# Performance work log

Hardware: AMD Instinct MI355X
Metric: run time of the kernel (lower is better)

The kernel has to match this reference:

```python
import jax, jax.numpy as jnp
import numpy as np

EMBED_DIM = 1024
NUM_HEADS = 16
HEAD_DIM = EMBED_DIM // NUM_HEADS


def setup_inputs() -> dict:
    key = jax.random.key(0)
    ks = jax.random.split(key, 5)
    s = 0.02
    return {
        "x": jax.random.normal(ks[0], (2, 2048, EMBED_DIM), dtype=jnp.float32),
        "w_qkv": jax.random.normal(ks[1], (EMBED_DIM, 3 * EMBED_DIM), dtype=jnp.float32) * s,
        "b_qkv": jnp.zeros((3 * EMBED_DIM,), dtype=jnp.float32),
        "w_out": jax.random.normal(ks[2], (EMBED_DIM, EMBED_DIM), dtype=jnp.float32) * s,
        "b_out": jnp.zeros((EMBED_DIM,), dtype=jnp.float32),
    }


def reference(x, w_qkv, b_qkv, w_out, b_out):
    B, T, C = x.shape
    qkv = x @ w_qkv + b_qkv                       # [B,T,3C]
    q, k, v = jnp.split(qkv, 3, axis=-1)
    # [B,T,C] -> [B,H,T,Dh]
    def heads(t):
        return t.reshape(B, T, NUM_HEADS, HEAD_DIM).transpose(0, 2, 1, 3)
    q, k, v = heads(q), heads(k), heads(v)
    scale = 1.0 / np.sqrt(HEAD_DIM).astype(np.float32)
    scores = jnp.einsum("bhqd,bhkd->bhqk", q, k) * scale  # [B,H,T,T]
    causal = jnp.tril(jnp.ones((T, T), dtype=bool))
    scores = jnp.where(causal[None, None], scores, -jnp.inf)
    attn = jax.nn.softmax(scores, axis=-1)
    out = jnp.einsum("bhqk,bhkd->bhqd", attn, v)  # [B,H,T,Dh]
    out = out.transpose(0, 2, 1, 3).reshape(B, T, C)
    return out @ w_out + b_out
```

## Files before the change

### kernel.cpp

```cpp
#include <hip/hip_runtime.h>

typedef unsigned short u16;
typedef unsigned int u32;
typedef __attribute__((ext_vector_type(2))) unsigned int u32x2;
typedef __attribute__((ext_vector_type(8))) short bf16x8;
typedef __attribute__((ext_vector_type(4))) float f32x4;
typedef __attribute__((ext_vector_type(16))) float f32x16;

#define TOK   4096
#define EMB   1024
#define NQKV  3072
#define TSEQ  2048
#define NH    16

__device__ __forceinline__ u16 f2b(float f) {
  union { float f; unsigned u; } v; v.f = f;
  unsigned r = v.u + 0x7FFFu + ((v.u >> 16) & 1u);
  return (u16)(r >> 16);
}

__device__ __forceinline__ u16 f2b_hu(float f) {
  return (u16)((__float_as_uint(f) + 0x8000u) >> 16);
}

__device__ __forceinline__ u32 pack_rn(float a, float b) {
  u32 ua = __float_as_uint(a) + 0x8000u;
  u32 ub = __float_as_uint(b) + 0x8000u;
  return __builtin_amdgcn_perm(ub, ua, 0x07060302u);
}

__device__ __forceinline__ f32x16 zero16() {
  f32x16 z;
#pragma unroll
  for (int i = 0; i < 16; i++) z[i] = 0.f;
  return z;
}

__device__ __forceinline__ void gload16(const void* g, void* l) {
  __builtin_amdgcn_global_load_lds((const __attribute__((address_space(1))) void*)g,
                                   (__attribute__((address_space(3))) void*)l, 16, 0, 0);
}


__global__ __launch_bounds__(256) void prep_kernel(const float* __restrict__ x,
                                                   u16* __restrict__ x_bf,
                                                   const float* __restrict__ w_qkv,
                                                   u16* __restrict__ wqkvT,
                                                   const float* __restrict__ w_out,
                                                   u16* __restrict__ woutT) {
  __shared__ u16 sm[64][65];
  int bid = blockIdx.x, tid = threadIdx.x;
  if (bid < 4096) {
    int i = bid * 256 + tid;
    float4 v = ((const float4*)x)[i];
    union { u16 us[4]; uint2 u2; } o;
    o.us[0] = f2b(v.x); o.us[1] = f2b(v.y); o.us[2] = f2b(v.z); o.us[3] = f2b(v.w);
    ((uint2*)x_bf)[i] = o.u2;
    return;
  }
  const float* src; u16* dst; int R, C, bx, by;
  if (bid < 4096 + 768) {
    int t = bid - 4096; bx = t % 48; by = t / 48;
    src = w_qkv; dst = wqkvT; R = EMB; C = NQKV;
  } else {
    int t = bid - 4096 - 768; bx = t & 15; by = t >> 4;
    src = w_out; dst = woutT; R = EMB; C = EMB;
  }
  int c0 = bx * 64, r0 = by * 64;
#pragma unroll
  for (int i = 0; i < 16; i++) {
    int idx = tid + i * 256;
    int r = idx >> 6, c = idx & 63;
    sm[r][c] = f2b(src[(size_t)(r0 + r) * C + c0 + c]);
  }
  __syncthreads();
  int cc2 = tid >> 2, rr0 = (tid & 3) * 16;
  union { u16 us[16]; uint4 v4[2]; } o;
#pragma unroll
  for (int j = 0; j < 16; j++) o.us[j] = sm[rr0 + j][cc2];
  *(uint4*)&dst[(size_t)(c0 + cc2) * R + r0 + rr0]     = o.v4[0];
  *(uint4*)&dst[(size_t)(c0 + cc2) * R + r0 + rr0 + 8] = o.v4[1];
}


template <int MODE, int TN, int CW, int CH>
__global__ __launch_bounds__(256) void gemm_bt(const u16* __restrict__ A,
                                               const u16* __restrict__ Bt,
                                               const float* __restrict__ bias,
                                               u16* __restrict__ qb, u16* __restrict__ kb,
                                               u16* __restrict__ vb, float* __restrict__ outp,
                                               int K, int N) {
  constexpr int CT = TN / 32;
  constexpr int RB = TN / 32;
  __shared__ u16 As[2][128][64];
  __shared__ u16 Bs[2][TN][64];
  int tid = threadIdx.x;
  int bx, by;
  if constexpr (CW > 0) {
    int bid = blockIdx.x;
    int xcd = bid & 7, idx = bid >> 3;
    bx = (xcd & 1) * CW + idx % CW;
    by = (xcd >> 1) * CH + idx / CW;
  } else {
    bx = blockIdx.x; by = blockIdx.y;
  }
  int m0 = by * 128, n0 = bx * TN;
  int lane = tid & 63, wid = tid >> 6;
  int wm = (wid >> 1) * 64;
  int wn = (wid & 1) * (TN / 2);
  int l15 = lane & 15, quad = lane >> 4;
  int srow = lane >> 3;
  int scol = (((lane & 7) ^ srow) * 8);

  f32x4 acc[4][CT];
#pragma unroll
  for (int i = 0; i < 4; i++)
#pragma unroll
    for (int j = 0; j < CT; j++) acc[i][j] = (f32x4){0.f, 0.f, 0.f, 0.f};

  const u16* Ag = A + (size_t)(m0 + wid * 32 + srow) * K + scol;
  const u16* Bg = Bt + (size_t)(n0 + wid * (TN / 4) + srow) * K + scol;

#pragma unroll
  for (int i = 0; i < 4; i++)
    gload16(Ag + (size_t)(i * 8) * K, &As[0][wid * 32 + i * 8][0]);
#pragma unroll
  for (int i = 0; i < RB; i++)
    gload16(Bg + (size_t)(i * 8) * K, &Bs[0][wid * (TN / 4) + i * 8][0]);
  __syncthreads();

  int cur = 0;
  for (int k0 = 0; k0 < K; k0 += 64) {
    if (k0 + 64 < K) {
      int kn = k0 + 64;
#pragma unroll
      for (int i = 0; i < 4; i++)
        gload16(Ag + (size_t)(i * 8) * K + kn, &As[cur ^ 1][wid * 32 + i * 8][0]);
#pragma unroll
      for (int i = 0; i < RB; i++)
        gload16(Bg + (size_t)(i * 8) * K + kn, &Bs[cur ^ 1][wid * (TN / 4) + i * 8][0]);
    }

#pragma unroll
    for (int ks = 0; ks < 2; ks++) {
      bf16x8 af[4], bfr[CT];
#pragma unroll
      for (int rt = 0; rt < 4; rt++)
        af[rt] = *(const bf16x8*)&As[cur][wm + rt * 16 + l15][((ks * 4 + quad) ^ (l15 & 7)) * 8];
#pragma unroll
      for (int ct = 0; ct < CT; ct++)
        bfr[ct] = *(const bf16x8*)&Bs[cur][wn + ct * 16 + l15][((ks * 4 + quad) ^ (l15 & 7)) * 8];
#pragma unroll
      for (int rt = 0; rt < 4; rt++)
#pragma unroll
        for (int ct = 0; ct < CT; ct++)
          acc[rt][ct] = __builtin_amdgcn_mfma_f32_16x16x32_bf16(bfr[ct], af[rt], acc[rt][ct], 0, 0, 0);
    }
    __syncthreads();
    cur ^= 1;
  }

#pragma unroll
  for (int rt = 0; rt < 4; rt++) {
#pragma unroll
    for (int ct = 0; ct < CT; ct++) {
      int m = m0 + wm + rt * 16 + l15;
      int nb = n0 + wn + ct * 16 + quad * 4;
      float4 b4 = *(const float4*)&bias[nb];
      float v0 = acc[rt][ct][0] + b4.x, v1 = acc[rt][ct][1] + b4.y;
      float v2 = acc[rt][ct][2] + b4.z, v3 = acc[rt][ct][3] + b4.w;
      if (MODE == 0) {
        int sel = nb >> 10;
        int c = nb & 1023;
        int h = c >> 6, d0 = c & 63;
        int b = m >> 11, t = m & 2047;
        if (sel == 2) {
          size_t vbase = ((((size_t)b * NH + h) * 64 + d0) * TSEQ) + t;
          vb[vbase]            = f2b_hu(v0);
          vb[vbase + TSEQ]     = f2b_hu(v1);
          vb[vbase + 2 * TSEQ] = f2b_hu(v2);
          vb[vbase + 3 * TSEQ] = f2b_hu(v3);
        } else {
          u16* dst = sel ? kb : qb;
          union { u32 u[2]; uint2 u2; } o;
          o.u[0] = pack_rn(v0, v1);
          o.u[1] = pack_rn(v2, v3);
          *(uint2*)&dst[((((size_t)b * NH + h) * TSEQ + t) << 6) + d0] = o.u2;
        }
      } else {
        float4 o = {v0, v1, v2, v3};
        *(float4*)&outp[(size_t)m * N + nb] = o;
      }
    }
  }
}


__global__ __launch_bounds__(256, 4) void attn_kernel(const u16* __restrict__ Qb,
                                                      const u16* __restrict__ Kb,
                                                      const u16* __restrict__ Vtb,
                                                      u16* __restrict__ O) {
  __shared__ u16 Ks[64][68];
  __shared__ u16 Vt[64][68];
  __shared__ float Cmb[2][16][64][2];
  __shared__ float Lmb[2][32];

  const float SCL = 0.18033688f;
  const float MOFF = 16.0f;

  int phys = blockIdx.x;
  int xcd = phys & 7;
  int cuL = (phys >> 3) & 31;
  int slot = phys >> 8;
  int bh = xcd * 4 + slot;
  int qt = (slot & 1) ? (31 - cuL) : cuL;

  int tid = threadIdx.x, lane = tid & 63, w = tid >> 6;
  int sub = w & 1, par = w >> 1;
  int l31 = lane & 31, h = lane >> 5;
  const size_t hoff = (size_t)bh * TSEQ * 64;

  int qw = qt * 64 + sub * 32;
  int qg = qw + l31;

  bf16x8 qf[4];
  {
    const u16* qp = Qb + hoff + (size_t)qg * 64 + h * 8;
#pragma unroll
    for (int s = 0; s < 4; s++) qf[s] = *(const bf16x8*)(qp + s * 16);
  }

  f32x16 acc[2];
  acc[0] = zero16(); acc[1] = zero16();
  float l_i = 0.f;

  int r = tid >> 2, cb = (tid & 3) * 16;
  bf16x8 kr0, kr1, vr0, vr1;
  {
    const u16* kg = Kb + hoff + (size_t)r * 64 + cb;
    const u16* vg = Vtb + hoff + (size_t)r * TSEQ + cb;
    kr0 = *(const bf16x8*)kg;       kr1 = *(const bf16x8*)(kg + 8);
    vr0 = *(const bf16x8*)vg;       vr1 = *(const bf16x8*)(vg + 8);
  }

  for (int kt = 0; kt <= qt; kt++) {
    __syncthreads();
    *(bf16x8*)&Ks[r][cb]     = kr0;
    *(bf16x8*)&Ks[r][cb + 8] = kr1;
    *(bf16x8*)&Vt[r][cb]     = vr0;
    *(bf16x8*)&Vt[r][cb + 8] = vr1;
    __syncthreads();
    if (kt < qt) {
      const u16* kg = Kb + hoff + (size_t)((kt + 1) * 64 + r) * 64 + cb;
      const u16* vg = Vtb + hoff + (size_t)r * TSEQ + (kt + 1) * 64 + cb;
      kr0 = *(const bf16x8*)kg;     kr1 = *(const bf16x8*)(kg + 8);
      vr0 = *(const bf16x8*)vg;     vr1 = *(const bf16x8*)(vg + 8);
    }

    int kbt = kt * 64 + par * 32;
    if (kbt <= qw + 31) {
      f32x16 sacc = zero16();
      __builtin_amdgcn_s_setprio(1);
#pragma unroll
      for (int s = 0; s < 4; s++) {
        bf16x8 kf = *(const bf16x8*)&Ks[par * 32 + l31][s * 16 + h * 8];
        sacc = __builtin_amdgcn_mfma_f32_32x32x16_bf16(kf, qf[s], sacc, 0, 0, 0);
      }
      __builtin_amdgcn_s_setprio(0);

      if (kbt + 31 > qw) {
#pragma unroll
        for (int rr = 0; rr < 16; rr++) {
          int key = kbt + (rr & 3) + 8 * (rr >> 2) + 4 * h;
          if (key > qg) sacc[rr] = -1e30f;
        }
      }

#pragma unroll
      for (int rr = 0; rr < 16; rr++) {
        float p = exp2f(__builtin_fmaf(sacc[rr], SCL, -MOFF));
        sacc[rr] = p;
        l_i += p;
      }

#pragma unroll
      for (int s2 = 0; s2 < 2; s2++) {
        u32 u0, u1, u2, u3;
        asm("v_cvt_pk_bf16_f32 %0, %1, %2" : "=v"(u0) : "v"(sacc[8 * s2 + 0]), "v"(sacc[8 * s2 + 1]));
        asm("v_cvt_pk_bf16_f32 %0, %1, %2" : "=v"(u1) : "v"(sacc[8 * s2 + 2]), "v"(sacc[8 * s2 + 3]));
        asm("v_cvt_pk_bf16_f32 %0, %1, %2" : "=v"(u2) : "v"(sacc[8 * s2 + 4]), "v"(sacc[8 * s2 + 5]));
        asm("v_cvt_pk_bf16_f32 %0, %1, %2" : "=v"(u3) : "v"(sacc[8 * s2 + 6]), "v"(sacc[8 * s2 + 7]));
        u32x2 r02 = __builtin_amdgcn_permlane32_swap(u0, u2, false, false);
        u32x2 r13 = __builtin_amdgcn_permlane32_swap(u1, u3, false, false);
        union { u32 d[4]; bf16x8 v; } pf;
        pf.d[0] = r02[0];
        pf.d[1] = r13[0];
        pf.d[2] = r02[1];
        pf.d[3] = r13[1];
        __builtin_amdgcn_s_setprio(1);
#pragma unroll
        for (int dt = 0; dt < 2; dt++) {
          bf16x8 vf = *(const bf16x8*)&Vt[dt * 32 + l31][par * 32 + s2 * 16 + h * 8];
          acc[dt] = __builtin_amdgcn_mfma_f32_32x32x16_bf16(vf, pf.v, acc[dt], 0, 0, 0);
        }
        __builtin_amdgcn_s_setprio(0);
      }
    }
  }

  l_i += __shfl_xor(l_i, 32);

  __syncthreads();
  if (par == 1) {
#pragma unroll
    for (int dt = 0; dt < 2; dt++)
#pragma unroll
      for (int pr = 0; pr < 8; pr++) {
        Cmb[sub][dt * 8 + pr][lane][0] = acc[dt][2 * pr];
        Cmb[sub][dt * 8 + pr][lane][1] = acc[dt][2 * pr + 1];
      }
    if (h == 0) Lmb[sub][l31] = l_i;
  }
  __syncthreads();
  if (par == 0) {
#pragma unroll
    for (int dt = 0; dt < 2; dt++)
#pragma unroll
      for (int pr = 0; pr < 8; pr++) {
        acc[dt][2 * pr]     += Cmb[sub][dt * 8 + pr][lane][0];
        acc[dt][2 * pr + 1] += Cmb[sub][dt * 8 + pr][lane][1];
      }
    float lt = l_i + Lmb[sub][l31];
    float inv = 1.0f / lt;

    int b = bh >> 4, head = bh & 15;
    size_t rowbase = ((size_t)b * TSEQ + qg) * 1024 + head * 64;
#pragma unroll
    for (int dt = 0; dt < 2; dt++)
#pragma unroll
      for (int G = 0; G < 4; G++) {
        union { u32 u[2]; uint2 u2; } o;
        o.u[0] = pack_rn(acc[dt][4 * G + 0] * inv, acc[dt][4 * G + 1] * inv);
        o.u[1] = pack_rn(acc[dt][4 * G + 2] * inv, acc[dt][4 * G + 3] * inv);
        *(uint2*)&O[rowbase + dt * 32 + G * 8 + 4 * h] = o.u2;
      }
  }
}


extern "C" void kernel_launch(void* const* d_in, const int* in_sizes, int n_in,
                              void* d_out, int out_size, void* d_ws, size_t ws_size,
                              hipStream_t stream) {
  (void)in_sizes; (void)n_in; (void)out_size; (void)ws_size;
  const float* x     = (const float*)d_in[0];
  const float* w_qkv = (const float*)d_in[1];
  const float* b_qkv = (const float*)d_in[2];
  const float* w_out = (const float*)d_in[3];
  const float* b_out = (const float*)d_in[4];
  float* out = (float*)d_out;

  char* p = (char*)d_ws;
  u16* x_bf  = (u16*)p; p += (size_t)TOK * EMB * 2;
  u16* wqkvT = (u16*)p; p += (size_t)NQKV * EMB * 2;
  u16* woutT = (u16*)p; p += (size_t)EMB * EMB * 2;
  u16* Qb    = (u16*)p; p += (size_t)32 * TSEQ * 64 * 2;
  u16* Kb    = (u16*)p; p += (size_t)32 * TSEQ * 64 * 2;
  u16* Vtb   = (u16*)p; p += (size_t)32 * TSEQ * 64 * 2;
  u16* attn_o = (u16*)p;

  prep_kernel<<<dim3(4096 + 768 + 256), 256, 0, stream>>>(x, x_bf, w_qkv, wqkvT, w_out, woutT);
  gemm_bt<0, 128, 12, 8><<<dim3(768), 256, 0, stream>>>(x_bf, wqkvT, b_qkv,
                                                        Qb, Kb, Vtb, nullptr, EMB, NQKV);
  attn_kernel<<<dim3(1024), 256, 0, stream>>>(Qb, Kb, Vtb, attn_o);
  gemm_bt<1, 64, 0, 0><<<dim3(EMB / 64, TOK / 128), 256, 0, stream>>>(attn_o, woutT, b_out,
                                                                      nullptr, nullptr, nullptr, out, EMB, EMB);
}
```

Baseline: 182.7 us.

## Double-buffer K/V tiles in LDS to drop one barrier per iteration

The attention kernel moves from a single LDS buffer for the K and V tiles to two buffers, unioned with the final combine scratch. Each iteration writes the next tile into the spare buffer and issues global loads two tiles ahead, so only one __syncthreads is needed per step. The row-sum accumulation is also split into four partial accumulators to shorten the dependent add chain. LDS use per block roughly doubles for the K/V part, which could limit occupancy under the 4-blocks-per-CU launch bound, and it keeps more registers live.

```diff
diff --git a/kernel.cpp b/kernel.cpp
--- a/kernel.cpp
+++ b/kernel.cpp
@@ -200,10 +200,10 @@
                                                       const u16* __restrict__ Kb,
                                                       const u16* __restrict__ Vtb,
                                                       u16* __restrict__ O) {
-  __shared__ u16 Ks[64][68];
-  __shared__ u16 Vt[64][68];
-  __shared__ float Cmb[2][16][64][2];
-  __shared__ float Lmb[2][32];
+  __shared__ union __align__(16) SM {
+    struct { u16 Ks[2][64][68]; u16 Vt[2][64][68]; } kv;
+    struct { float Cmb[2][16][64][2]; float Lmb[2][32]; } cb;
+  } sm;
 
   const float SCL = 0.18033688f;
   const float MOFF = 16.0f;
@@ -232,27 +232,40 @@
 
   f32x16 acc[2];
   acc[0] = zero16(); acc[1] = zero16();
-  float l_i = 0.f;
+  float lp0 = 0.f, lp1 = 0.f, lp2 = 0.f, lp3 = 0.f;
 
   int r = tid >> 2, cb = (tid & 3) * 16;
   bf16x8 kr0, kr1, vr0, vr1;
+
   {
     const u16* kg = Kb + hoff + (size_t)r * 64 + cb;
     const u16* vg = Vtb + hoff + (size_t)r * TSEQ + cb;
     kr0 = *(const bf16x8*)kg;       kr1 = *(const bf16x8*)(kg + 8);
     vr0 = *(const bf16x8*)vg;       vr1 = *(const bf16x8*)(vg + 8);
+    *(bf16x8*)&sm.kv.Ks[0][r][cb]     = kr0;
+    *(bf16x8*)&sm.kv.Ks[0][r][cb + 8] = kr1;
+    *(bf16x8*)&sm.kv.Vt[0][r][cb]     = vr0;
+    *(bf16x8*)&sm.kv.Vt[0][r][cb + 8] = vr1;
+    if (qt >= 1) {
+      const u16* kg1 = Kb + hoff + (size_t)(64 + r) * 64 + cb;
+      const u16* vg1 = Vtb + hoff + (size_t)r * TSEQ + 64 + cb;
+      kr0 = *(const bf16x8*)kg1;    kr1 = *(const bf16x8*)(kg1 + 8);
+      vr0 = *(const bf16x8*)vg1;    vr1 = *(const bf16x8*)(vg1 + 8);
+    }
   }
 
   for (int kt = 0; kt <= qt; kt++) {
     __syncthreads();
-    *(bf16x8*)&Ks[r][cb]     = kr0;
-    *(bf16x8*)&Ks[r][cb + 8] = kr1;
-    *(bf16x8*)&Vt[r][cb]     = vr0;
-    *(bf16x8*)&Vt[r][cb + 8] = vr1;
-    __syncthreads();
-    if (kt < qt) {
-      const u16* kg = Kb + hoff + (size_t)((kt + 1) * 64 + r) * 64 + cb;
-      const u16* vg = Vtb + hoff + (size_t)r * TSEQ + (kt + 1) * 64 + cb;
+    int cur = kt & 1;
+    if (kt + 1 <= qt) {
+      *(bf16x8*)&sm.kv.Ks[cur ^ 1][r][cb]     = kr0;
+      *(bf16x8*)&sm.kv.Ks[cur ^ 1][r][cb + 8] = kr1;
+      *(bf16x8*)&sm.kv.Vt[cur ^ 1][r][cb]     = vr0;
+      *(bf16x8*)&sm.kv.Vt[cur ^ 1][r][cb + 8] = vr1;
+    }
+    if (kt + 2 <= qt) {
+      const u16* kg = Kb + hoff + (size_t)((kt + 2) * 64 + r) * 64 + cb;
+      const u16* vg = Vtb + hoff + (size_t)r * TSEQ + (kt + 2) * 64 + cb;
       kr0 = *(const bf16x8*)kg;     kr1 = *(const bf16x8*)(kg + 8);
       vr0 = *(const bf16x8*)vg;     vr1 = *(const bf16x8*)(vg + 8);
     }
@@ -263,7 +276,7 @@
       __builtin_amdgcn_s_setprio(1);
 #pragma unroll
       for (int s = 0; s < 4; s++) {
-        bf16x8 kf = *(const bf16x8*)&Ks[par * 32 + l31][s * 16 + h * 8];
+        bf16x8 kf = *(const bf16x8*)&sm.kv.Ks[cur][par * 32 + l31][s * 16 + h * 8];
         sacc = __builtin_amdgcn_mfma_f32_32x32x16_bf16(kf, qf[s], sacc, 0, 0, 0);
       }
       __builtin_amdgcn_s_setprio(0);
@@ -280,7 +293,10 @@
       for (int rr = 0; rr < 16; rr++) {
         float p = exp2f(__builtin_fmaf(sacc[rr], SCL, -MOFF));
         sacc[rr] = p;
-        l_i += p;
+        if ((rr & 3) == 0)      lp0 += p;
+        else if ((rr & 3) == 1) lp1 += p;
+        else if ((rr & 3) == 2) lp2 += p;
+        else                    lp3 += p;
       }
 
 #pragma unroll
@@ -300,7 +316,7 @@
         __builtin_amdgcn_s_setprio(1);
 #pragma unroll
         for (int dt = 0; dt < 2; dt++) {
-          bf16x8 vf = *(const bf16x8*)&Vt[dt * 32 + l31][par * 32 + s2 * 16 + h * 8];
+          bf16x8 vf = *(const bf16x8*)&sm.kv.Vt[cur][dt * 32 + l31][par * 32 + s2 * 16 + h * 8];
           acc[dt] = __builtin_amdgcn_mfma_f32_32x32x16_bf16(vf, pf.v, acc[dt], 0, 0, 0);
         }
         __builtin_amdgcn_s_setprio(0);
@@ -308,6 +324,7 @@
     }
   }
 
+  float l_i = (lp0 + lp1) + (lp2 + lp3);
   l_i += __shfl_xor(l_i, 32);
 
   __syncthreads();
@@ -316,10 +333,10 @@
     for (int dt = 0; dt < 2; dt++)
 #pragma unroll
       for (int pr = 0; pr < 8; pr++) {
-        Cmb[sub][dt * 8 + pr][lane][0] = acc[dt][2 * pr];
-        Cmb[sub][dt * 8 + pr][lane][1] = acc[dt][2 * pr + 1];
-      }
-    if (h == 0) Lmb[sub][l31] = l_i;
+        sm.cb.Cmb[sub][dt * 8 + pr][lane][0] = acc[dt][2 * pr];
+        sm.cb.Cmb[sub][dt * 8 + pr][lane][1] = acc[dt][2 * pr + 1];
+      }
+    if (h == 0) sm.cb.Lmb[sub][l31] = l_i;
   }
   __syncthreads();
   if (par == 0) {
@@ -327,10 +344,10 @@
     for (int dt = 0; dt < 2; dt++)
 #pragma unroll
       for (int pr = 0; pr < 8; pr++) {
-        acc[dt][2 * pr]     += Cmb[sub][dt * 8 + pr][lane][0];
-        acc[dt][2 * pr + 1] += Cmb[sub][dt * 8 + pr][lane][1];
-      }
-    float lt = l_i + Lmb[sub][l31];
+        acc[dt][2 * pr]     += sm.cb.Cmb[sub][dt * 8 + pr][lane][0];
+        acc[dt][2 * pr + 1] += sm.cb.Cmb[sub][dt * 8 + pr][lane][1];
+      }
+    float lt = l_i + sm.cb.Lmb[sub][l31];
     float inv = 1.0f / lt;
 
     int b = bh >> 4, head = bh & 15;
```

After: 184.2 us. Within noise of the previous version (+0.8%).
